# Optimization experiments

Hardware: AMD Instinct MI355X
Metric: run time of the kernel (lower is better)

The kernel has to match this reference:

```python
import jax, jax.numpy as jnp
import numpy as np

B, S, K, N = 4, 2048, 4096, 4096


def setup_inputs() -> dict:
    key = jax.random.key(0)
    k1, k2, k3, k4 = jax.random.split(key, 4)
    x = jax.random.normal(k1, (B, S, K), dtype=jnp.float32)
    # int8 quantized weight values in [-128, 127], stored as int32 (jax-friendly container)
    qw = jax.random.randint(k2, (N, K), -128, 128, dtype=jnp.int32)
    # per-tensor scale: amax/127 style scalar
    sw = (jax.random.uniform(k3, (), dtype=jnp.float32) * 0.02 + 0.001)
    bias = jax.random.normal(k4, (N,), dtype=jnp.float32)
    return {"x": x, "qw": qw, "sw": sw, "bias": bias}


def reference(x, qw, sw, bias):
    # per_tensor_matmul: dequantize weight to fp32 with scalar scale, fp32 GEMM, cast back, add bias
    x_dtype = x.dtype
    w = qw.astype(jnp.float32) * sw          # [N, K] dequantized
    y = jnp.einsum('bsk,nk->bsn', x.astype(jnp.float32), w).astype(x_dtype)
    y = y + bias                              # [B, S, N]
    return y
```

## Files before the change

kernel.cpp:

```cpp
#include <hip/hip_runtime.h>
#include <stdint.h>

#define MDIM 8192
#define NDIM 4096
#define KDIM 4096

#define BM 256
#define BN 256
#define BK 128
#define NKT (KDIM / BK)

typedef __attribute__((ext_vector_type(4)))  int i32x4;

#define AS1 __attribute__((address_space(1)))
#define AS3 __attribute__((address_space(3)))

__device__ __forceinline__ int clamp127(int v) {
    return v > 127 ? 127 : (v < -127 ? -127 : v);
}

__global__ __launch_bounds__(256) void quant_x(
        const float* __restrict__ x, const float* __restrict__ sw,
        int8_t* __restrict__ Aq, float* __restrict__ scales) {
    const int row = blockIdx.x;
    const int t   = threadIdx.x;
    const float4* px = (const float4*)(x + (size_t)row * KDIM);

    float4 v[4];
#pragma unroll
    for (int j = 0; j < 4; j++) v[j] = px[t + 256 * j];

    float a = 0.f;
#pragma unroll
    for (int j = 0; j < 4; j++) {
        a = fmaxf(a, fabsf(v[j].x)); a = fmaxf(a, fabsf(v[j].y));
        a = fmaxf(a, fabsf(v[j].z)); a = fmaxf(a, fabsf(v[j].w));
    }
#pragma unroll
    for (int off = 32; off >= 1; off >>= 1)
        a = fmaxf(a, __shfl_xor(a, off));
    __shared__ float red[4];
    if ((t & 63) == 0) red[t >> 6] = a;
    __syncthreads();
    const float amax = fmaxf(fmaxf(red[0], red[1]), fmaxf(red[2], red[3]));
    const float inv  = (amax > 0.f) ? (127.0f / amax) : 0.f;
    if (t == 0) scales[row] = (amax * (1.0f / 127.0f)) * (*sw);

    int* out32 = (int*)(Aq + (size_t)row * KDIM);
#pragma unroll
    for (int j = 0; j < 4; j++) {
        int b0 = clamp127(__float2int_rn(v[j].x * inv));
        int b1 = clamp127(__float2int_rn(v[j].y * inv));
        int b2 = clamp127(__float2int_rn(v[j].z * inv));
        int b3 = clamp127(__float2int_rn(v[j].w * inv));
        out32[t + 256 * j] = (b0 & 255) | ((b1 & 255) << 8) | ((b2 & 255) << 16) | ((b3 & 255) << 24);
    }
}

__global__ __launch_bounds__(256) void cvt_w(const int* __restrict__ qw, int8_t* __restrict__ Bq) {
    const long i = (long)blockIdx.x * 256 + threadIdx.x;
    int4 a = ((const int4*)qw)[i];
    ((int*)Bq)[i] = (a.x & 255) | ((a.y & 255) << 8) | ((a.z & 255) << 16) | ((a.w & 255) << 24);
}


#define BAR()    do { asm volatile("" ::: "memory"); __builtin_amdgcn_s_barrier(); asm volatile("" ::: "memory"); } while (0)
#define LGKM0()  asm volatile("s_waitcnt lgkmcnt(0)" ::: "memory")
#define WAITV(n) asm volatile("s_waitcnt vmcnt(" #n ")" ::: "memory")

#define STAGE_A(buf, h, kt) do { \
    __builtin_amdgcn_global_load_lds((AS1 const void*)(gA + (size_t)((h) * 128) * KDIM + (kt) * 128), \
        (AS3 void*)(sA + (buf) * 32768 + (h) * 16384 + sdst), 16, 0, 0); \
    __builtin_amdgcn_global_load_lds((AS1 const void*)(gA + (size_t)((h) * 128 + 64) * KDIM + (kt) * 128), \
        (AS3 void*)(sA + (buf) * 32768 + (h) * 16384 + 8192 + sdst), 16, 0, 0); \
} while (0)

#define STAGE_B(buf, h, kt) do { \
    __builtin_amdgcn_global_load_lds((AS1 const void*)(gB + (size_t)((h) * 128) * KDIM + (kt) * 128), \
        (AS3 void*)(sB + (buf) * 32768 + (h) * 16384 + sdst), 16, 0, 0); \
    __builtin_amdgcn_global_load_lds((AS1 const void*)(gB + (size_t)((h) * 128 + 64) * KDIM + (kt) * 128), \
        (AS3 void*)(sB + (buf) * 32768 + (h) * 16384 + 8192 + sdst), 16, 0, 0); \
} while (0)

#define READ_A0(buf) do { \
    _Pragma("unroll") for (int mi = 0; mi < 4; ++mi) \
    _Pragma("unroll") for (int ks = 0; ks < 2; ++ks) \
        aF0[mi][ks] = *(const i32x4*)(sA + (buf) * 32768 + rbA + mi * 2048 + co[ks]); \
} while (0)

#define READ_A1a(buf) do { \
    _Pragma("unroll") for (int mi = 0; mi < 2; ++mi) \
    _Pragma("unroll") for (int ks = 0; ks < 2; ++ks) \
        aF1[mi][ks] = *(const i32x4*)(sA + (buf) * 32768 + rbA + (4 + mi) * 2048 + co[ks]); \
} while (0)

#define READ_A1b(buf) do { \
    _Pragma("unroll") for (int mi = 2; mi < 4; ++mi) \
    _Pragma("unroll") for (int ks = 0; ks < 2; ++ks) \
        aF1[mi][ks] = *(const i32x4*)(sA + (buf) * 32768 + rbA + (4 + mi) * 2048 + co[ks]); \
} while (0)

#define READ_B01(buf) do { \
    _Pragma("unroll") for (int ni = 0; ni < 2; ++ni) \
    _Pragma("unroll") for (int ks = 0; ks < 2; ++ks) \
        bF01[ni][ks] = *(const i32x4*)(sB + (buf) * 32768 + rbB + ni * 2048 + co[ks]); \
} while (0)

#define READ_B23(buf) do { \
    _Pragma("unroll") for (int ni = 0; ni < 2; ++ni) \
    _Pragma("unroll") for (int ks = 0; ks < 2; ++ks) \
        bF23[ni][ks] = *(const i32x4*)(sB + (buf) * 32768 + rbB + (2 + ni) * 2048 + co[ks]); \
} while (0)

#define MMA_(AF, accbase, BF, nhofs) do { \
    __builtin_amdgcn_s_setprio(1); \
    _Pragma("unroll") for (int ks = 0; ks < 2; ++ks) \
    _Pragma("unroll") for (int mi = 0; mi < 4; ++mi) \
    _Pragma("unroll") for (int nj = 0; nj < 2; ++nj) \
        acc[(accbase) + mi][(nhofs) + nj] = __builtin_amdgcn_mfma_i32_16x16x64_i8( \
            AF[mi][ks], BF[nj][ks], acc[(accbase) + mi][(nhofs) + nj], 0, 0, 0); \
    __builtin_amdgcn_s_setprio(0); \
} while (0)

__global__ __launch_bounds__(512, 2) void gemm_bt_i8(
        const int8_t* __restrict__ A,
        const int8_t* __restrict__ Bm,
        const float* __restrict__ scales,
        const float* __restrict__ bias,
        float* __restrict__ C)
{
    __shared__ __align__(16) int8_t sA[2 * BM * BK];
    __shared__ __align__(16) int8_t sB[2 * BN * BK];

    const int tid  = threadIdx.x;
    const int wave = tid >> 6;
    const int lane = tid & 63;
    const int wr   = wave >> 2;
    const int wc   = wave & 3;
    const int lr   = lane & 15;
    const int lg   = lane >> 4;

    const int orig = blockIdx.y * 16 + blockIdx.x;
    const int nu   = (orig & 7) * 64 + (orig >> 3);
    const int m0   = (nu >> 4) * BM;
    const int n0   = (nu & 15) * BN;

    const int trow = tid >> 3;
    const int slog = (tid & 7) ^ ((tid >> 3) & 7);
    const int8_t* gA = A  + (size_t)(m0 + trow) * KDIM + slog * 16;
    const int8_t* gB = Bm + (size_t)(n0 + trow) * KDIM + slog * 16;
    const int sdst = tid * 16;

    const int f3 = lr & 7;
    const int rbA = (wr * 128 + lr) * BK;
    const int rbB = (wc * 64  + lr) * BK;
    int co[2];
#pragma unroll
    for (int ks = 0; ks < 2; ++ks) co[ks] = (((ks << 2) | lg) ^ f3) << 4;

    i32x4 acc[8][4];
#pragma unroll
    for (int mi = 0; mi < 8; ++mi)
#pragma unroll
        for (int ni = 0; ni < 4; ++ni)
#pragma unroll
            for (int r = 0; r < 4; ++r) acc[mi][ni][r] = 0;

    i32x4 aF0[4][2];
    i32x4 aF1[4][2];
    i32x4 bF01[2][2];
    i32x4 bF23[2][2];

    STAGE_A(0, 0, 0); STAGE_A(0, 1, 0);
    STAGE_B(0, 0, 0); STAGE_B(0, 1, 0);
    STAGE_A(1, 0, 1); STAGE_A(1, 1, 1);
    WAITV(4);
    BAR();
    READ_A0(0); READ_B01(0);

#pragma unroll 1
    for (int it = 0; it < NKT / 2 - 1; ++it) {
        const int e = 2 * it;
        READ_B23(0); READ_A1a(0);  MMA_(aF0, 0, bF01, 0);  STAGE_B(1, 0, e + 1);  BAR();
        READ_A1b(0);               MMA_(aF0, 0, bF23, 2);  STAGE_B(1, 1, e + 1);  LGKM0(); WAITV(4); BAR();
        READ_A0(1);                MMA_(aF1, 4, bF01, 0);  STAGE_A(0, 0, e + 2);  WAITV(2); BAR();
        READ_B01(1);               MMA_(aF1, 4, bF23, 2);  STAGE_A(0, 1, e + 2);  BAR();
        READ_B23(1); READ_A1a(1);  MMA_(aF0, 0, bF01, 0);  STAGE_B(0, 0, e + 2);  BAR();
        READ_A1b(1);               MMA_(aF0, 0, bF23, 2);  STAGE_B(0, 1, e + 2);  LGKM0(); WAITV(4); BAR();
        READ_A0(0);                MMA_(aF1, 4, bF01, 0);  STAGE_A(1, 0, e + 3);  WAITV(2); BAR();
        READ_B01(0);               MMA_(aF1, 4, bF23, 2);  STAGE_A(1, 1, e + 3);  BAR();
    }

    READ_B23(0); READ_A1a(0);  MMA_(aF0, 0, bF01, 0);  STAGE_B(1, 0, 31);  BAR();
    READ_A1b(0);               MMA_(aF0, 0, bF23, 2);  STAGE_B(1, 1, 31);  LGKM0(); WAITV(4); BAR();
    READ_A0(1);                MMA_(aF1, 4, bF01, 0);  WAITV(0); BAR();
    READ_B01(1);               MMA_(aF1, 4, bF23, 2);  BAR();
    READ_B23(1); READ_A1a(1);  MMA_(aF0, 0, bF01, 0);  BAR();
    READ_A1b(1);               MMA_(aF0, 0, bF23, 2);
    MMA_(aF1, 4, bF01, 0);
    MMA_(aF1, 4, bF23, 2);

#pragma unroll
    for (int mi = 0; mi < 8; ++mi) {
        const int row_base = m0 + wr * 128 + mi * 16 + lg * 4;
        float sc[4];
#pragma unroll
        for (int r = 0; r < 4; ++r) sc[r] = scales[row_base + r];
#pragma unroll
        for (int ni = 0; ni < 4; ++ni) {
            const int col = n0 + wc * 64 + ni * 16 + lr;
            const float bc = bias[col];
#pragma unroll
            for (int r = 0; r < 4; ++r)
                C[(size_t)(row_base + r) * NDIM + col] = (float)acc[mi][ni][r] * sc[r] + bc;
        }
    }
}

__global__ void gemm_naive_f32(const float* __restrict__ x, const int* __restrict__ qw,
                               const float* __restrict__ sw, const float* __restrict__ bias,
                               float* __restrict__ out) {
    size_t id = (size_t)blockIdx.x * blockDim.x + threadIdx.x;
    if (id >= (size_t)MDIM * NDIM) return;
    int m = (int)(id / NDIM);
    int n = (int)(id % NDIM);
    const float* xr = x + (size_t)m * KDIM;
    const int*   wr = qw + (size_t)n * KDIM;
    float acc = 0.f;
    for (int k = 0; k < KDIM; k++) acc += xr[k] * (float)wr[k];
    out[id] = acc * (*sw) + bias[n];
}

extern "C" void kernel_launch(void* const* d_in, const int* in_sizes, int n_in,
                              void* d_out, int out_size, void* d_ws, size_t ws_size,
                              hipStream_t stream) {
    const float* x    = (const float*)d_in[0];
    const int*   qw   = (const int*)d_in[1];
    const float* sw   = (const float*)d_in[2];
    const float* bias = (const float*)d_in[3];
    float* out = (float*)d_out;

    const size_t needA = (size_t)MDIM * KDIM;
    const size_t needB = (size_t)NDIM * KDIM;
    const size_t needS = (size_t)MDIM * sizeof(float);

    if (ws_size >= needA + needB + needS) {
        int8_t* Aq = (int8_t*)d_ws;
        int8_t* Bq = Aq + needA;
        float*  scales = (float*)(Bq + needB);

        quant_x<<<MDIM, 256, 0, stream>>>(x, sw, Aq, scales);
        const long nw4 = (long)NDIM * KDIM / 4;
        cvt_w<<<(int)(nw4 / 256), 256, 0, stream>>>(qw, Bq);

        dim3 grid(NDIM / BN, MDIM / BM);
        gemm_bt_i8<<<grid, 512, 0, stream>>>(Aq, Bq, scales, bias, out);
    } else {
        size_t total = (size_t)MDIM * NDIM;
        gemm_naive_f32<<<(total + 255) / 256, 256, 0, stream>>>(x, qw, sw, bias, out);
    }
}
```

Measured before the change: 391.4 us.

## Restructure int8 GEMM main loop to two barriers per K-tile with full-tile prefetch

The K-loop pipeline is rescheduled so both A and B for the next-next K-tile are staged together after a single barrier per half-iteration. This replaces the finer interleaving that used four barriers per tile with partial vmcnt waits. The prologue now prefetches both stages of A and B before starting. The aim is fewer workgroup barriers and less synchronization stall, at the cost of WAITV(0) full drains that may expose global load latency.

```diff
diff --git a/kernel.cpp b/kernel.cpp
--- a/kernel.cpp
+++ b/kernel.cpp
@@ -174,28 +174,32 @@
     STAGE_A(0, 0, 0); STAGE_A(0, 1, 0);
     STAGE_B(0, 0, 0); STAGE_B(0, 1, 0);
     STAGE_A(1, 0, 1); STAGE_A(1, 1, 1);
-    WAITV(4);
+    STAGE_B(1, 0, 1); STAGE_B(1, 1, 1);
+    WAITV(8);
     BAR();
     READ_A0(0); READ_B01(0);
 
 #pragma unroll 1
     for (int it = 0; it < NKT / 2 - 1; ++it) {
         const int e = 2 * it;
-        READ_B23(0); READ_A1a(0);  MMA_(aF0, 0, bF01, 0);  STAGE_B(1, 0, e + 1);  BAR();
-        READ_A1b(0);               MMA_(aF0, 0, bF23, 2);  STAGE_B(1, 1, e + 1);  LGKM0(); WAITV(4); BAR();
-        READ_A0(1);                MMA_(aF1, 4, bF01, 0);  STAGE_A(0, 0, e + 2);  WAITV(2); BAR();
-        READ_B01(1);               MMA_(aF1, 4, bF23, 2);  STAGE_A(0, 1, e + 2);  BAR();
-        READ_B23(1); READ_A1a(1);  MMA_(aF0, 0, bF01, 0);  STAGE_B(0, 0, e + 2);  BAR();
-        READ_A1b(1);               MMA_(aF0, 0, bF23, 2);  STAGE_B(0, 1, e + 2);  LGKM0(); WAITV(4); BAR();
-        READ_A0(0);                MMA_(aF1, 4, bF01, 0);  STAGE_A(1, 0, e + 3);  WAITV(2); BAR();
-        READ_B01(0);               MMA_(aF1, 4, bF23, 2);  STAGE_A(1, 1, e + 3);  BAR();
-    }
-
-    READ_B23(0); READ_A1a(0);  MMA_(aF0, 0, bF01, 0);  STAGE_B(1, 0, 31);  BAR();
-    READ_A1b(0);               MMA_(aF0, 0, bF23, 2);  STAGE_B(1, 1, 31);  LGKM0(); WAITV(4); BAR();
-    READ_A0(1);                MMA_(aF1, 4, bF01, 0);  WAITV(0); BAR();
-    READ_B01(1);               MMA_(aF1, 4, bF23, 2);  BAR();
-    READ_B23(1); READ_A1a(1);  MMA_(aF0, 0, bF01, 0);  BAR();
+        READ_B23(0); READ_A1a(0);  MMA_(aF0, 0, bF01, 0);
+        READ_A1b(0);               MMA_(aF0, 0, bF23, 2);
+        LGKM0(); WAITV(0); BAR();
+        READ_A0(1);                MMA_(aF1, 4, bF01, 0);  STAGE_A(0, 0, e + 2); STAGE_B(0, 0, e + 2);
+        READ_B01(1);               MMA_(aF1, 4, bF23, 2);  STAGE_A(0, 1, e + 2); STAGE_B(0, 1, e + 2);
+        READ_B23(1); READ_A1a(1);  MMA_(aF0, 0, bF01, 0);
+        READ_A1b(1);               MMA_(aF0, 0, bF23, 2);
+        LGKM0(); WAITV(0); BAR();
+        READ_A0(0);                MMA_(aF1, 4, bF01, 0);  STAGE_A(1, 0, e + 3); STAGE_B(1, 0, e + 3);
+        READ_B01(0);               MMA_(aF1, 4, bF23, 2);  STAGE_A(1, 1, e + 3); STAGE_B(1, 1, e + 3);
+    }
+
+    READ_B23(0); READ_A1a(0);  MMA_(aF0, 0, bF01, 0);
+    READ_A1b(0);               MMA_(aF0, 0, bF23, 2);
+    LGKM0(); WAITV(0); BAR();
+    READ_A0(1);                MMA_(aF1, 4, bF01, 0);
+    READ_B01(1);               MMA_(aF1, 4, bF23, 2);
+    READ_B23(1); READ_A1a(1);  MMA_(aF0, 0, bF01, 0);
     READ_A1b(1);               MMA_(aF0, 0, bF23, 2);
     MMA_(aF1, 4, bF01, 0);
     MMA_(aF1, 4, bF23, 2);
```

Measured after the change: 403.3 us. 3.0% more time.
